# Kernel optimization log

Measured on AMD Instinct MI355X. Metric: run time of the kernel, lower is better.

## Reference

```python
import jax, jax.numpy as jnp
import numpy as np

MIN_NORM = 1e-15
BALL_EPS = 4e-3   # HGCN float32 projection epsilon
MAX_NORM = 1e6    # manifold.max_norm used in torch.clamp(max=...)
C = 1.0           # c_in == c_out
N, E, D = 50000, 800000, 128


def artanh(x):
    return jnp.arctanh(jnp.clip(x, -1.0 + 1e-7, 1.0 - 1e-7))


def _norm(x):
    return jnp.clip(jnp.linalg.norm(x, axis=-1, keepdims=True), MIN_NORM)


def proj(x, c):
    # clip points to stay inside the Poincare ball of curvature c
    sc = c ** 0.5
    n = _norm(x)
    maxn = (1.0 - BALL_EPS) / sc
    return jnp.where(n > maxn, x / n * maxn, x)


def expmap0(u, c):
    sc = c ** 0.5
    n = _norm(u)
    return jnp.tanh(sc * n) * u / (sc * n)


def logmap0(p, c):
    sc = c ** 0.5
    n = _norm(p)
    return artanh(sc * n) * p / (sc * n)


def mobius_matvec(w, x, c):
    sc = c ** 0.5
    xn = _norm(x)
    mx = x @ w.T                      # [N, D_out]
    mxn = _norm(mx)
    res = jnp.tanh(mxn / xn * artanh(sc * xn)) * mx / (mxn * sc)
    zero = jnp.all(mx == 0, axis=-1, keepdims=True)
    return jnp.where(zero, jnp.zeros_like(res), res)


def mobius_add(x, y, c):
    x2 = jnp.sum(x * x, -1, keepdims=True)
    y2 = jnp.sum(y * y, -1, keepdims=True)
    xy = jnp.sum(x * y, -1, keepdims=True)
    num = (1 + 2 * c * xy + c * y2) * x + (1 - c * x2) * y
    den = 1 + 2 * c * xy + c * c * x2 * y2
    return num / jnp.clip(den, MIN_NORM)


def setup_inputs() -> dict:
    key = jax.random.key(0)
    k1, k2, k3, k4, k5 = jax.random.split(key, 5)
    # valid Poincare-ball points: expmap0 of small tangent vectors
    xt = 0.1 * jax.random.normal(k1, (N, D), jnp.float32)
    x = proj(expmap0(xt, C), C)
    edge_row = jax.random.randint(k2, (E,), 0, N)
    edge_col = jax.random.randint(k3, (E,), 0, N)
    adj_val = jax.random.uniform(k4, (E,), jnp.float32) / 16.0  # ~normalized adjacency weights
    weight = jax.random.normal(k5, (D, D), jnp.float32) * (2.0 / D) ** 0.5  # xavier, gain sqrt(2)
    bias = jnp.full((D,), 1e-4, jnp.float32)  # init.constant_(bias, 0.0001)
    return {"x": x, "adj_val": adj_val, "weight": weight, "bias": bias,
            "edge_row": edge_row, "edge_col": edge_col}


def reference(x, adj_val, weight, bias, edge_row, edge_col):
    c = C
    # ---- HypLinear (eval mode: no dropout) ----
    h = proj(mobius_matvec(weight, x, c), c)
    hyp_bias = proj(expmap0(bias[None, :], c), c)  # proj_tan0 is identity on the ball
    h = proj(mobius_add(h, hyp_bias, c), c)
    # ---- HypAgg (spmm path) ----
    x_tangent = logmap0(h, c)                                     # [N, D]
    msgs = adj_val[:, None] * x_tangent[edge_col]                 # [E, D] gather
    support_t = jax.ops.segment_sum(msgs, edge_row, num_segments=N)
    support_t = jnp.minimum(support_t, MAX_NORM)                  # clamp(max=max_norm)
    h = proj(expmap0(support_t, c), c)
    # ---- HypAct (relu in tangent space at origin) ----
    xt = jnp.minimum(jax.nn.relu(logmap0(h, c)), MAX_NORM)
    out = expmap0(xt, c)  # c_out == c_in; HypAct does not re-project
    return out
```

## Files before the change

kernel.cpp:

```cpp
#include <hip/hip_runtime.h>

#define D 128
#define MAXN 0.996f
#define MINN 1e-15f
#define ARTANH_MAX (1.0f - 1e-7f)
#define MAX_NORM 1e6f

typedef unsigned int uint;
typedef unsigned short ushort;
typedef __bf16 bf16x8 __attribute__((ext_vector_type(8)));
typedef float f32x4 __attribute__((ext_vector_type(4)));

__device__ __forceinline__ float wave_sum(float v) {
#pragma unroll
    for (int o = 32; o > 0; o >>= 1) v += __shfl_xor(v, o, 64);
    return v;
}

__device__ __forceinline__ float quad_sum(float v) {
    v += __shfl_xor(v, 16, 64);
    v += __shfl_xor(v, 32, 64);
    return v;
}

__device__ __forceinline__ float artanh_clip(float x) {
    x = fminf(fmaxf(x, -ARTANH_MAX), ARTANH_MAX);
    return 0.5f * logf((1.0f + x) / (1.0f - x));
}

__device__ __forceinline__ ushort f2bf(float f) {
    uint u = __float_as_uint(f);
    return (ushort)((u + 0x7fffu + ((u >> 16) & 1u)) >> 16);
}

__device__ __forceinline__ uint pk2(float a, float b) {
    return (uint)f2bf(a) | ((uint)f2bf(b) << 16);
}

__global__ __launch_bounds__(256)
void wconv_kernel(const float* __restrict__ W, ushort* __restrict__ WB)
{
    int i = blockIdx.x * 256 + threadIdx.x;
    WB[i] = f2bf(W[i]);
}

__global__ __launch_bounds__(256)
void gemm_mfma_kernel(const float* __restrict__ X, const ushort* __restrict__ WB,
                      const float* __restrict__ bias, ushort* __restrict__ XT, int N)
{
    const int wid = threadIdx.x >> 6;
    const int l   = threadIdx.x & 63;
    const int m0  = (blockIdx.x * 4 + wid) * 16;
    if (m0 >= N) return;
    const int lr = l & 15;
    const int kg = l >> 4;
    const int row = m0 + lr;
    const int rowc = row < N ? row : N - 1;

    const float* xp = X + (size_t)rowc * D + kg * 4;
    bf16x8 bfr[4];
    float xsq = 0.f;
#pragma unroll
    for (int ks = 0; ks < 4; ++ks) {
        float4 v0 = *(const float4*)(xp + ks * 32);
        float4 v1 = *(const float4*)(xp + ks * 32 + 16);
        xsq += v0.x*v0.x + v0.y*v0.y + v0.z*v0.z + v0.w*v0.w
             + v1.x*v1.x + v1.y*v1.y + v1.z*v1.z + v1.w*v1.w;
        uint4 bq = make_uint4(pk2(v0.x, v0.y), pk2(v0.z, v0.w),
                              pk2(v1.x, v1.y), pk2(v1.z, v1.w));
        bfr[ks] = __builtin_bit_cast(bf16x8, bq);
    }
    xsq = quad_sum(xsq);

    float4 bb[8];
    float bsq = 0.f;
#pragma unroll
    for (int t = 0; t < 8; ++t) {
        bb[t] = *(const float4*)(bias + t * 16 + kg * 4);
        bsq += bb[t].x*bb[t].x + bb[t].y*bb[t].y + bb[t].z*bb[t].z + bb[t].w*bb[t].w;
    }
    bsq = quad_sum(bsq);
    float bn  = fmaxf(sqrtf(bsq), MINN);
    float bt  = tanhf(bn);
    float bps = (bt > MAXN) ? MAXN / fmaxf(bt, MINN) : 1.0f;
    float bsc = bt / bn * bps;
    float bhn = fminf(fmaxf(bt * bps, MINN), MAXN);
    float y2  = bhn * bhn;

    f32x4 acc[8];
#pragma unroll
    for (int t = 0; t < 8; ++t) acc[t] = (f32x4){0.f, 0.f, 0.f, 0.f};
#pragma unroll
    for (int ks = 0; ks < 4; ++ks) {
#pragma unroll
        for (int t = 0; t < 8; ++t) {
            const ushort* wrow = WB + (size_t)(t * 16 + lr) * D + ks * 32 + kg * 4;
            uint2 wlo = *(const uint2*)(wrow);
            uint2 whi = *(const uint2*)(wrow + 16);
            uint4 wv = make_uint4(wlo.x, wlo.y, whi.x, whi.y);
            bf16x8 af = __builtin_bit_cast(bf16x8, wv);
            acc[t] = __builtin_amdgcn_mfma_f32_16x16x32_bf16(af, bfr[ks], acc[t], 0, 0, 0);
        }
    }

    float sacc = 0.f, sab = 0.f;
#pragma unroll
    for (int t = 0; t < 8; ++t) {
        sacc += acc[t][0]*acc[t][0] + acc[t][1]*acc[t][1] + acc[t][2]*acc[t][2] + acc[t][3]*acc[t][3];
        sab  += acc[t][0]*bb[t].x + acc[t][1]*bb[t].y + acc[t][2]*bb[t].z + acc[t][3]*bb[t].w;
    }
    sacc = quad_sum(sacc);
    sab  = quad_sum(sab);

    float xn  = fmaxf(sqrtf(xsq), MINN);
    float mxn = fmaxf(sqrtf(sacc), MINN);
    float t1  = tanhf(mxn / xn * artanh_clip(xn));
    float s1  = t1 / mxn;
    float ps1 = (t1 > MAXN) ? MAXN / fmaxf(t1, MINN) : 1.0f;
    float s1p = s1 * ps1;
    float rn  = fminf(fmaxf(t1, MINN), MAXN);
    float x2  = rn * rn;
    float mxb = bsc * sab;
    float xy  = s1p * mxb;
    float ca  = 1.0f + 2.0f * xy + y2;
    float cb  = 1.0f - x2;
    float den = fmaxf(1.0f + 2.0f * xy + x2 * y2, MINN);
    float alpha = ca * s1p / den;
    float beta  = cb / den;
    float hn2 = alpha * alpha * sacc + 2.0f * alpha * beta * mxb + beta * beta * y2;
    float hn  = fmaxf(sqrtf(hn2), MINN);
    float ps2 = (hn > MAXN) ? MAXN / hn : 1.0f;
    float hnc = fmaxf(fminf(hn, MAXN), MINN);
    float ls  = artanh_clip(hnc) / hnc;
    float F   = ls * ps2;
    float A = F * alpha, Bc = F * beta * bsc;

    if (row < N) {
        ushort* op = XT + (size_t)row * D + kg * 4;
#pragma unroll
        for (int t = 0; t < 8; ++t) {
            uint2 o = make_uint2(pk2(A * acc[t][0] + Bc * bb[t].x, A * acc[t][1] + Bc * bb[t].y),
                                 pk2(A * acc[t][2] + Bc * bb[t].z, A * acc[t][3] + Bc * bb[t].w));
            *(uint2*)(op + t * 16) = o;
        }
    }
}

__global__ __launch_bounds__(256)
void hist_kernel(const int* __restrict__ erow, int* __restrict__ cnt,
                 int* __restrict__ rank, int E)
{
    int e = blockIdx.x * 256 + threadIdx.x;
    if (e < E) rank[e] = atomicAdd(&cnt[erow[e]], 1);
}

__global__ __launch_bounds__(256)
void scan1_kernel(const int* __restrict__ cnt, int* __restrict__ offs,
                  int* __restrict__ bsum, int N)
{
    __shared__ int wsum[4];
    int t = threadIdx.x;
    int base = blockIdx.x * 1024 + t * 4;
    int v[4];
#pragma unroll
    for (int j = 0; j < 4; ++j) v[j] = (base + j < N) ? cnt[base + j] : 0;
    int tt = v[0] + v[1] + v[2] + v[3];
    int incl = tt;
#pragma unroll
    for (int o = 1; o < 64; o <<= 1) {
        int n = __shfl_up(incl, o, 64);
        if ((t & 63) >= o) incl += n;
    }
    if ((t & 63) == 63) wsum[t >> 6] = incl;
    __syncthreads();
    int wbase = 0;
    for (int w = 0; w < (t >> 6); ++w) wbase += wsum[w];
    int ex = wbase + incl - tt;
#pragma unroll
    for (int j = 0; j < 4; ++j) {
        if (base + j < N) offs[base + j] = ex;
        ex += v[j];
    }
    if (t == 255) bsum[blockIdx.x] = wbase + incl;
}

__global__ __launch_bounds__(64)
void scan2_kernel(int* __restrict__ bsum, int nb)
{
    int l = threadIdx.x;
    int v = (l < nb) ? bsum[l] : 0;
    int incl = v;
#pragma unroll
    for (int o = 1; o < 64; o <<= 1) {
        int n = __shfl_up(incl, o, 64);
        if (l >= o) incl += n;
    }
    if (l < nb) bsum[l] = incl - v;
}

__global__ __launch_bounds__(256)
void fill_kernel(const int* __restrict__ erow, const int* __restrict__ ecol,
                 const float* __restrict__ adj, const int* __restrict__ rank,
                 const int* __restrict__ offs, const int* __restrict__ bsum,
                 uint* __restrict__ bpack, int E)
{
    int e = blockIdx.x * 256 + threadIdx.x;
    if (e >= E) return;
    int r = erow[e];
    int p = offs[r] + bsum[r >> 10] + rank[e];
    bpack[p] = ((uint)ecol[e] << 16) | (uint)f2bf(adj[e]);
}

__global__ __launch_bounds__(256)
void gather_kernel(const ushort* __restrict__ XT, const uint* __restrict__ bpack,
                   const int* __restrict__ offs, const int* __restrict__ bsum,
                   const int* __restrict__ cnt, float* __restrict__ OUT, int N)
{
    int row = blockIdx.x * 4 + (threadIdx.x >> 6);
    int lane = threadIdx.x & 63;
    if (row >= N) return;
    int start = offs[row] + bsum[row >> 10];
    int end = start + cnt[row];
    const uint* xtw = (const uint*)XT;
    float ax[8] = {0.f, 0.f, 0.f, 0.f, 0.f, 0.f, 0.f, 0.f};
    float ay[8] = {0.f, 0.f, 0.f, 0.f, 0.f, 0.f, 0.f, 0.f};
    int i = start;
    for (; i + 7 < end; i += 8) {
        uint4 qa = *(const uint4*)(bpack + i);
        uint4 qb = *(const uint4*)(bpack + i + 4);
        uint q[8] = {qa.x, qa.y, qa.z, qa.w, qb.x, qb.y, qb.z, qb.w};
#pragma unroll
        for (int j = 0; j < 8; ++j) {
            uint u = xtw[(size_t)(q[j] >> 16) * 64 + lane];
            float v = __uint_as_float(q[j] << 16);
            ax[j] += v * __uint_as_float(u << 16);
            ay[j] += v * __uint_as_float(u & 0xffff0000u);
        }
    }
    for (; i + 3 < end; i += 4) {
        uint4 qa = *(const uint4*)(bpack + i);
        uint q[4] = {qa.x, qa.y, qa.z, qa.w};
#pragma unroll
        for (int j = 0; j < 4; ++j) {
            uint u = xtw[(size_t)(q[j] >> 16) * 64 + lane];
            float v = __uint_as_float(q[j] << 16);
            ax[j] += v * __uint_as_float(u << 16);
            ay[j] += v * __uint_as_float(u & 0xffff0000u);
        }
    }
    for (; i < end; ++i) {
        uint q = bpack[i];
        float v = __uint_as_float(q << 16);
        uint u = xtw[(size_t)(q >> 16) * 64 + lane];
        ax[0] += v * __uint_as_float(u << 16);
        ay[0] += v * __uint_as_float(u & 0xffff0000u);
    }
    float tx = ((ax[0] + ax[1]) + (ax[2] + ax[3])) + ((ax[4] + ax[5]) + (ax[6] + ax[7]));
    float ty = ((ay[0] + ay[1]) + (ay[2] + ay[3])) + ((ay[4] + ay[5]) + (ay[6] + ay[7]));
    tx = fminf(tx, MAX_NORM);
    ty = fminf(ty, MAX_NORM);
    float nt = fmaxf(sqrtf(wave_sum(tx * tx + ty * ty)), MINN);
    float es = tanhf(nt) / nt;
    float h0 = es * tx, h1 = es * ty;
    float hn = fmaxf(sqrtf(wave_sum(h0 * h0 + h1 * h1)), MINN);
    if (hn > MAXN) { float f = MAXN / hn; h0 *= f; h1 *= f; }
    float hn2 = fmaxf(sqrtf(wave_sum(h0 * h0 + h1 * h1)), MINN);
    float ls = artanh_clip(hn2) / hn2;
    float u0 = fminf(fmaxf(ls * h0, 0.0f), MAX_NORM);
    float u1 = fminf(fmaxf(ls * h1, 0.0f), MAX_NORM);
    float un = fmaxf(sqrtf(wave_sum(u0 * u0 + u1 * u1)), MINN);
    float os = tanhf(un) / un;
    float2 o; o.x = os * u0; o.y = os * u1;
    ((float2*)(OUT + (size_t)row * D))[lane] = o;
}

extern "C" void kernel_launch(void* const* d_in, const int* in_sizes, int n_in,
                              void* d_out, int out_size, void* d_ws, size_t ws_size,
                              hipStream_t stream)
{
    const float* x    = (const float*)d_in[0];
    const float* adj  = (const float*)d_in[1];
    const float* W    = (const float*)d_in[2];
    const float* bias = (const float*)d_in[3];
    const int*   erow = (const int*)d_in[4];
    const int*   ecol = (const int*)d_in[5];
    float* out = (float*)d_out;
    const int N = in_sizes[0] / D;
    const int E = in_sizes[1];

    char* p = (char*)d_ws;
    size_t off = 0;
    auto alloc = [&](size_t bytes) {
        char* r = p + off;
        off = (off + bytes + 255) & ~(size_t)255;
        return r;
    };
    ushort* xt  = (ushort*)alloc((size_t)N * D * sizeof(ushort));
    ushort* wb  = (ushort*)alloc((size_t)D * D * sizeof(ushort));
    int*   cnt  = (int*)  alloc((size_t)N * sizeof(int));
    int*   offs = (int*)  alloc((size_t)N * sizeof(int));
    int*   bsum = (int*)  alloc(256 * sizeof(int));
    int*   rank = (int*)  alloc((size_t)E * sizeof(int));
    uint*  bpack= (uint*) alloc((size_t)E * sizeof(uint));
    (void)ws_size;

    hipMemsetAsync(cnt, 0, (size_t)N * sizeof(int), stream);
    wconv_kernel<<<(D * D) / 256, 256, 0, stream>>>(W, wb);
    gemm_mfma_kernel<<<(N + 63) / 64, 256, 0, stream>>>(x, wb, bias, xt, N);
    hist_kernel<<<(E + 255) / 256, 256, 0, stream>>>(erow, cnt, rank, E);
    int nb = (N + 1023) / 1024;
    scan1_kernel<<<nb, 256, 0, stream>>>(cnt, offs, bsum, N);
    scan2_kernel<<<1, 64, 0, stream>>>(bsum, nb);
    fill_kernel<<<(E + 255) / 256, 256, 0, stream>>>(erow, ecol, adj, rank, offs, bsum, bpack, E);
    gather_kernel<<<(N + 3) / 4, 256, 0, stream>>>(xt, bpack, offs, bsum, cnt, out, N);
}
```

Before: 145.4 us.

## Pre-swizzle W into MFMA fragments, vectorize edge kernels, and simplify gather epilogue

The weight is converted once into per-lane bf16 MFMA fragments, so the GEMM kernel loads each A operand as one coalesced 16-byte read instead of two strided 8-byte reads. The GEMM now uses 128-thread blocks and issues its weight loads before the bias math. The histogram and fill kernels each handle four edges per thread with int4/float4 loads, plus a scalar tail loop. The gather epilogue computes the projection and logmap analytically from the tanh norm, dropping two wave reductions. Together these cut memory transactions and reduction overhead, at the cost of a serial tail in one thread and a slightly different rounding order.

```diff
diff --git a/kernel.cpp b/kernel.cpp
--- a/kernel.cpp
+++ b/kernel.cpp
@@ -38,19 +38,26 @@
 }
 
 __global__ __launch_bounds__(256)
-void wconv_kernel(const float* __restrict__ W, ushort* __restrict__ WB)
-{
-    int i = blockIdx.x * 256 + threadIdx.x;
-    WB[i] = f2bf(W[i]);
-}
-
-__global__ __launch_bounds__(256)
-void gemm_mfma_kernel(const float* __restrict__ X, const ushort* __restrict__ WB,
+void wconv_kernel(const float* __restrict__ W, uint4* __restrict__ WF)
+{
+    int idx = blockIdx.x * 256 + threadIdx.x;
+    int l = idx & 63, rest = idx >> 6;
+    int t = rest & 7, ks = rest >> 3;
+    int lr = l & 15, kg = l >> 4;
+    const float* wrow = W + (size_t)(t * 16 + lr) * D + ks * 32 + kg * 4;
+    float4 lo = *(const float4*)(wrow);
+    float4 hi = *(const float4*)(wrow + 16);
+    WF[idx] = make_uint4(pk2(lo.x, lo.y), pk2(lo.z, lo.w),
+                         pk2(hi.x, hi.y), pk2(hi.z, hi.w));
+}
+
+__global__ __launch_bounds__(128)
+void gemm_mfma_kernel(const float* __restrict__ X, const uint4* __restrict__ WF,
                       const float* __restrict__ bias, ushort* __restrict__ XT, int N)
 {
     const int wid = threadIdx.x >> 6;
     const int l   = threadIdx.x & 63;
-    const int m0  = (blockIdx.x * 4 + wid) * 16;
+    const int m0  = (blockIdx.x * 2 + wid) * 16;
     if (m0 >= N) return;
     const int lr = l & 15;
     const int kg = l >> 4;
@@ -72,6 +79,20 @@
     }
     xsq = quad_sum(xsq);
 
+    f32x4 acc[8];
+#pragma unroll
+    for (int t = 0; t < 8; ++t) acc[t] = (f32x4){0.f, 0.f, 0.f, 0.f};
+#pragma unroll
+    for (int ks = 0; ks < 4; ++ks) {
+        uint4 wv[8];
+#pragma unroll
+        for (int t = 0; t < 8; ++t) wv[t] = WF[(ks * 8 + t) * 64 + l];
+#pragma unroll
+        for (int t = 0; t < 8; ++t)
+            acc[t] = __builtin_amdgcn_mfma_f32_16x16x32_bf16(
+                __builtin_bit_cast(bf16x8, wv[t]), bfr[ks], acc[t], 0, 0, 0);
+    }
+
     float4 bb[8];
     float bsq = 0.f;
 #pragma unroll
@@ -86,22 +107,6 @@
     float bsc = bt / bn * bps;
     float bhn = fminf(fmaxf(bt * bps, MINN), MAXN);
     float y2  = bhn * bhn;
-
-    f32x4 acc[8];
-#pragma unroll
-    for (int t = 0; t < 8; ++t) acc[t] = (f32x4){0.f, 0.f, 0.f, 0.f};
-#pragma unroll
-    for (int ks = 0; ks < 4; ++ks) {
-#pragma unroll
-        for (int t = 0; t < 8; ++t) {
-            const ushort* wrow = WB + (size_t)(t * 16 + lr) * D + ks * 32 + kg * 4;
-            uint2 wlo = *(const uint2*)(wrow);
-            uint2 whi = *(const uint2*)(wrow + 16);
-            uint4 wv = make_uint4(wlo.x, wlo.y, whi.x, whi.y);
-            bf16x8 af = __builtin_bit_cast(bf16x8, wv);
-            acc[t] = __builtin_amdgcn_mfma_f32_16x16x32_bf16(af, bfr[ks], acc[t], 0, 0, 0);
-        }
-    }
 
     float sacc = 0.f, sab = 0.f;
 #pragma unroll
@@ -150,8 +155,20 @@
 void hist_kernel(const int* __restrict__ erow, int* __restrict__ cnt,
                  int* __restrict__ rank, int E)
 {
-    int e = blockIdx.x * 256 + threadIdx.x;
-    if (e < E) rank[e] = atomicAdd(&cnt[erow[e]], 1);
+    int e4 = blockIdx.x * 256 + threadIdx.x;
+    int E4 = E >> 2;
+    if (e4 < E4) {
+        int4 r = ((const int4*)erow)[e4];
+        int4 k;
+        k.x = atomicAdd(&cnt[r.x], 1);
+        k.y = atomicAdd(&cnt[r.y], 1);
+        k.z = atomicAdd(&cnt[r.z], 1);
+        k.w = atomicAdd(&cnt[r.w], 1);
+        ((int4*)rank)[e4] = k;
+    }
+    if (e4 == 0) {
+        for (int i = E4 * 4; i < E; ++i) rank[i] = atomicAdd(&cnt[erow[i]], 1);
+    }
 }
 
 __global__ __launch_bounds__(256)
@@ -204,11 +221,24 @@
                  const int* __restrict__ offs, const int* __restrict__ bsum,
                  uint* __restrict__ bpack, int E)
 {
-    int e = blockIdx.x * 256 + threadIdx.x;
-    if (e >= E) return;
-    int r = erow[e];
-    int p = offs[r] + bsum[r >> 10] + rank[e];
-    bpack[p] = ((uint)ecol[e] << 16) | (uint)f2bf(adj[e]);
+    int e4 = blockIdx.x * 256 + threadIdx.x;
+    int E4 = E >> 2;
+    if (e4 < E4) {
+        int4   r = ((const int4*)erow)[e4];
+        int4   c = ((const int4*)ecol)[e4];
+        float4 a = ((const float4*)adj)[e4];
+        int4   k = ((const int4*)rank)[e4];
+        bpack[offs[r.x] + bsum[r.x >> 10] + k.x] = ((uint)c.x << 16) | (uint)f2bf(a.x);
+        bpack[offs[r.y] + bsum[r.y >> 10] + k.y] = ((uint)c.y << 16) | (uint)f2bf(a.y);
+        bpack[offs[r.z] + bsum[r.z >> 10] + k.z] = ((uint)c.z << 16) | (uint)f2bf(a.z);
+        bpack[offs[r.w] + bsum[r.w >> 10] + k.w] = ((uint)c.w << 16) | (uint)f2bf(a.w);
+    }
+    if (e4 == 0) {
+        for (int i = E4 * 4; i < E; ++i) {
+            int r = erow[i];
+            bpack[offs[r] + bsum[r >> 10] + rank[i]] = ((uint)ecol[i] << 16) | (uint)f2bf(adj[i]);
+        }
+    }
 }
 
 __global__ __launch_bounds__(256)
@@ -260,14 +290,14 @@
     tx = fminf(tx, MAX_NORM);
     ty = fminf(ty, MAX_NORM);
     float nt = fmaxf(sqrtf(wave_sum(tx * tx + ty * ty)), MINN);
-    float es = tanhf(nt) / nt;
-    float h0 = es * tx, h1 = es * ty;
-    float hn = fmaxf(sqrtf(wave_sum(h0 * h0 + h1 * h1)), MINN);
-    if (hn > MAXN) { float f = MAXN / hn; h0 *= f; h1 *= f; }
-    float hn2 = fmaxf(sqrtf(wave_sum(h0 * h0 + h1 * h1)), MINN);
-    float ls = artanh_clip(hn2) / hn2;
-    float u0 = fminf(fmaxf(ls * h0, 0.0f), MAX_NORM);
-    float u1 = fminf(fmaxf(ls * h1, 0.0f), MAX_NORM);
+    float th = tanhf(nt);
+    float es = th / nt;
+    float pf = (th > MAXN) ? MAXN / th : 1.0f;
+    float hnc = fmaxf(fminf(th, MAXN), MINN);
+    float ls = artanh_clip(hnc) / hnc;
+    float su = ls * pf * es;
+    float u0 = fminf(fmaxf(su * tx, 0.0f), MAX_NORM);
+    float u1 = fminf(fmaxf(su * ty, 0.0f), MAX_NORM);
     float un = fmaxf(sqrtf(wave_sum(u0 * u0 + u1 * u1)), MINN);
     float os = tanhf(un) / un;
     float2 o; o.x = os * u0; o.y = os * u1;
@@ -296,7 +326,7 @@
         return r;
     };
     ushort* xt  = (ushort*)alloc((size_t)N * D * sizeof(ushort));
-    ushort* wb  = (ushort*)alloc((size_t)D * D * sizeof(ushort));
+    uint4*  wf  = (uint4*) alloc(2048 * sizeof(uint4));
     int*   cnt  = (int*)  alloc((size_t)N * sizeof(int));
     int*   offs = (int*)  alloc((size_t)N * sizeof(int));
     int*   bsum = (int*)  alloc(256 * sizeof(int));
@@ -305,12 +335,13 @@
     (void)ws_size;
 
     hipMemsetAsync(cnt, 0, (size_t)N * sizeof(int), stream);
-    wconv_kernel<<<(D * D) / 256, 256, 0, stream>>>(W, wb);
-    gemm_mfma_kernel<<<(N + 63) / 64, 256, 0, stream>>>(x, wb, bias, xt, N);
-    hist_kernel<<<(E + 255) / 256, 256, 0, stream>>>(erow, cnt, rank, E);
+    wconv_kernel<<<8, 256, 0, stream>>>(W, wf);
+    gemm_mfma_kernel<<<(N + 31) / 32, 128, 0, stream>>>(x, wf, bias, xt, N);
+    int E4 = E >> 2;
+    hist_kernel<<<(E4 + 255) / 256, 256, 0, stream>>>(erow, cnt, rank, E);
     int nb = (N + 1023) / 1024;
     scan1_kernel<<<nb, 256, 0, stream>>>(cnt, offs, bsum, N);
     scan2_kernel<<<1, 64, 0, stream>>>(bsum, nb);
-    fill_kernel<<<(E + 255) / 256, 256, 0, stream>>>(erow, ecol, adj, rank, offs, bsum, bpack, E);
+    fill_kernel<<<(E4 + 255) / 256, 256, 0, stream>>>(erow, ecol, adj, rank, offs, bsum, bpack, E);
     gather_kernel<<<(N + 3) / 4, 256, 0, stream>>>(xt, bpack, offs, bsum, cnt, out, N);
 }
```

After: 119.1 us. -18.1%, faster.
